# Optimization experiments

Measured on AMD Instinct MI355X. Metric: run time of the kernel, lower is better.

Reference implementation:

```python
import jax, jax.numpy as jnp
import numpy as np
from jax import lax

STRIDE = 2  # down_sample_stride
MATMUL_NORM = True


def maxpool2d_5d(x, s):
    # x: [B, T, C, H, W]; kernel=s, stride=s, padding=(s-1)//2 == 0 for s=2
    return lax.reduce_window(
        x, -jnp.inf, lax.max,
        window_dimensions=(1, 1, 1, s, s),
        window_strides=(1, 1, 1, s, s),
        padding='VALID')


def setup_inputs() -> dict:
    key = jax.random.key(0)
    k1, k2, k3, k4 = jax.random.split(key, 4)
    B, T, Ck, Cv, H, W = 2, 4, 64, 256, 64, 64
    return {
        'memory_keys': jax.random.normal(k1, (B, T, Ck, H, W), jnp.float32),
        'memory_values': jax.random.normal(k2, (B, T, Cv, H, W), jnp.float32),
        'query_key': jax.random.normal(k3, (B, Ck, H, W), jnp.float32),
        'query_value': jax.random.normal(k4, (B, Cv, H, W), jnp.float32),
    }


def reference(memory_keys, memory_values, query_key, query_value):
    B, T, Ck, oH, oW = memory_keys.shape
    Cv = memory_values.shape[2]
    # down-sample memory bank (max pool, stride 2, no padding)
    mk = maxpool2d_5d(memory_keys, STRIDE)   # [B,T,Ck,h,w]
    mv = maxpool2d_5d(memory_values, STRIDE) # [B,T,Cv,h,w]
    h, w = mk.shape[-2], mk.shape[-1]
    M = T * h * w
    N = oH * oH  # code uses ori_height*ori_height (square assumed)
    # permute(0,2,1,3,4).view(B,Ck,M).permute(0,2,1) -> [B, M, Ck]
    mk = mk.transpose(0, 2, 1, 3, 4).reshape(B, Ck, M).transpose(0, 2, 1)
    qk = query_key.reshape(B, Ck, N)
    attn = jnp.einsum('bmc,bcn->bmn', mk, qk)  # [B, M, N]
    if MATMUL_NORM:
        attn = attn * (Ck ** -0.5)
    attn = jax.nn.softmax(attn, axis=1)  # softmax over memory positions
    mv = mv.transpose(0, 2, 1, 3, 4).reshape(B, Cv, M)
    memory = jnp.einsum('bcm,bmn->bcn', mv, attn).reshape(B, Cv, oH, oW)
    return jnp.concatenate([query_value, memory], axis=1)  # [B, 2*Cv, H, W]
```

## Files before the change

### kernel.cpp

```cpp
#include <hip/hip_runtime.h>
#include <hip/hip_bf16.h>

typedef unsigned short u16;
typedef unsigned int   u32;
typedef __attribute__((ext_vector_type(8))) short  bf16x8;
typedef __attribute__((ext_vector_type(4))) float  floatx4;

#define NB 2
#define NT 4
#define CK 64
#define CV 256
#define HH 64
#define WW 64
#define MM 4096
#define NN 4096
#define SCALE 0.125f
#define SHIFT 4.0f
#define OUT_B 2097152
#define MSPLIT 2
#define MHALF 2048
#define ITERS 16

__device__ __forceinline__ u16 f2b(float f) {
    __hip_bfloat16 h = __float2bfloat16(f);
    union { __hip_bfloat16 h; u16 u; } v; v.h = h; return v.u;
}


#define KTOT (NB*MM*CK)
__global__ void pool_kv(const float* __restrict__ mk, const float* __restrict__ mv,
                        u16* __restrict__ pk, u16* __restrict__ vt) {
    int e = blockIdx.x * 256 + threadIdx.x;
    if (e < KTOT) {
        int m = e & 4095; int c = (e >> 12) & 63; int b = e >> 18;
        int ww = m & 31, hh = (m >> 5) & 31, t = m >> 10;
        const float* s = mk + ((size_t)(((b*NT + t)*CK + c)*HH + 2*hh))*WW + 2*ww;
        pk[((size_t)b*MM + m)*CK + c] =
            f2b(fmaxf(fmaxf(s[0], s[1]), fmaxf(s[WW], s[WW+1])));
    } else {
        int e2 = e - KTOT;
        int m = e2 & 4095; int c = (e2 >> 12) & 255; int b = e2 >> 20;
        int ww = m & 31, hh = (m >> 5) & 31, t = m >> 10;
        const float* s = mv + ((size_t)(((b*NT + t)*CV + c)*HH + 2*hh))*WW + 2*ww;
        vt[((size_t)b*CV + c)*MM + m] =
            f2b(fmaxf(fmaxf(s[0], s[1]), fmaxf(s[WW], s[WW+1])));
    }
}

__launch_bounds__(512)
__global__ void attn_mfma(const u16* __restrict__ pk, const u16* __restrict__ vt,
                          const float* __restrict__ qk,
                          float* __restrict__ part, float* __restrict__ sums) {
    const int ntile = blockIdx.x, b = blockIdx.y, ms = blockIdx.z;
    const int tid = threadIdx.x, w = tid >> 6, l = tid & 63;
    const int lrow = l & 15, quad = l >> 4;
    const int n0 = ntile * 64;
    const int m0 = ms * MHALF;

    __shared__ u16  P[64 * 128];
    __shared__ float sums_s[8][64];

    bf16x8 qf[2][4];
    const float* qb = qk + (size_t)b * CK * NN;
    #pragma unroll
    for (int cc = 0; cc < 2; ++cc)
        #pragma unroll
        for (int t = 0; t < 4; ++t) {
            int n = n0 + t*16 + lrow;
            #pragma unroll
            for (int i = 0; i < 8; ++i) {
                int c = cc*32 + quad*8 + i;
                qf[cc][t][i] = (short)f2b(qb[(size_t)c*NN + n]);
            }
        }

    const u16* pkb = pk + (size_t)b * MM * CK;
    const u16* vtb = vt + (size_t)b * CV * MM;

    floatx4 oacc[2][4];
    #pragma unroll
    for (int j = 0; j < 2; ++j)
        #pragma unroll
        for (int t = 0; t < 4; ++t)
            oacc[j][t] = (floatx4){0.f, 0.f, 0.f, 0.f};
    float sacc[4] = {0.f, 0.f, 0.f, 0.f};

    const int sw = lrow << 1;

    for (int it = 0; it < ITERS; ++it) {
        const int mbase = m0 + it * 128;

        const u16* kp = pkb + (size_t)(mbase + w*16 + lrow)*CK + quad*8;
        bf16x8 kf0 = *(const bf16x8*)(kp);
        bf16x8 kf1 = *(const bf16x8*)(kp + 32);

        bf16x8 vf[4][2];
        #pragma unroll
        for (int j = 0; j < 2; ++j) {
            const u16* vp = vtb + (size_t)(w*32 + j*16 + lrow)*MM + mbase + quad*8;
            vf[0][j] = *(const bf16x8*)(vp);
            vf[1][j] = *(const bf16x8*)(vp + 32);
            vf[2][j] = *(const bf16x8*)(vp + 64);
            vf[3][j] = *(const bf16x8*)(vp + 96);
        }

        #pragma unroll
        for (int t = 0; t < 4; ++t) {
            floatx4 s = __builtin_amdgcn_mfma_f32_16x16x32_bf16(
                            kf0, qf[0][t], (floatx4){0.f,0.f,0.f,0.f}, 0, 0, 0);
            s = __builtin_amdgcn_mfma_f32_16x16x32_bf16(kf1, qf[1][t], s, 0, 0, 0);
            float p0 = __expf(s[0]*SCALE - SHIFT);
            float p1 = __expf(s[1]*SCALE - SHIFT);
            float p2 = __expf(s[2]*SCALE - SHIFT);
            float p3 = __expf(s[3]*SCALE - SHIFT);
            sacc[t] += (p0 + p1) + (p2 + p3);
            u32 d0 = (u32)f2b(p0) | ((u32)f2b(p1) << 16);
            u32 d1 = (u32)f2b(p2) | ((u32)f2b(p3) << 16);
            int n_l = t*16 + lrow;
            int cb  = (w << 2) + quad;
            *(uint2*)&P[n_l*128 + ((cb ^ sw) << 2)] = make_uint2(d0, d1);
        }
        __syncthreads();

        #pragma unroll
        for (int cc = 0; cc < 4; ++cc) {
            bf16x8 pf[4];
            #pragma unroll
            for (int t = 0; t < 4; ++t) {
                int n_l = t*16 + lrow;
                int cb  = (cc << 3) + (quad << 1);
                pf[t] = *(const bf16x8*)&P[n_l*128 + ((cb ^ sw) << 2)];
            }
            #pragma unroll
            for (int j = 0; j < 2; ++j)
                #pragma unroll
                for (int t = 0; t < 4; ++t)
                    oacc[j][t] = __builtin_amdgcn_mfma_f32_16x16x32_bf16(
                                     vf[cc][j], pf[t], oacc[j][t], 0, 0, 0);
        }
        __syncthreads();
    }

    #pragma unroll
    for (int t = 0; t < 4; ++t) {
        float v = sacc[t];
        v += __shfl_xor(v, 16, 64);
        v += __shfl_xor(v, 32, 64);
        if (l < 16) sums_s[w][t*16 + l] = v;
    }
    __syncthreads();

    float* pb = part + ((size_t)((ms*NB + b)*64 + ntile)) * (256*64);
    #pragma unroll
    for (int j = 0; j < 2; ++j)
        #pragma unroll
        for (int t = 0; t < 4; ++t)
            #pragma unroll
            for (int r = 0; r < 4; ++r) {
                int c = w*32 + j*16 + quad*4 + r;
                int n = t*16 + lrow;
                pb[c*64 + n] = oacc[j][t][r];
            }
    if (tid < 64) {
        float sv = 0.f;
        #pragma unroll
        for (int ww2 = 0; ww2 < 8; ++ww2) sv += sums_s[ww2][tid];
        sums[((size_t)((ms*NB + b)*64 + ntile))*64 + tid] = sv;
    }
}

__global__ void epilogue(const float* __restrict__ part, const float* __restrict__ sums,
                         const float4* __restrict__ qv, float* __restrict__ out) {
    int e = blockIdx.x * 256 + threadIdx.x;
    if (e < 524288) {
        int b = e >> 18; int ru = e & 262143;
        ((float4*)out)[(size_t)b*(OUT_B/4) + ru] = qv[e];
    } else {
        int e4 = e - 524288;
        int nl4   = e4 & 15;
        int ntile = (e4 >> 4) & 63;
        int c     = (e4 >> 10) & 255;
        int b     = e4 >> 18;
        size_t t0 = (size_t)(0*NB + b)*64 + ntile;
        size_t t1 = (size_t)(1*NB + b)*64 + ntile;
        const float4* p4 = (const float4*)part;
        const float4* s4 = (const float4*)sums;
        float4 u0 = p4[t0*4096 + c*16 + nl4];
        float4 u1 = p4[t1*4096 + c*16 + nl4];
        float4 d0 = s4[t0*16 + nl4];
        float4 d1 = s4[t1*16 + nl4];
        float4 r;
        r.x = (u0.x + u1.x) / (d0.x + d1.x);
        r.y = (u0.y + u1.y) / (d0.y + d1.y);
        r.z = (u0.z + u1.z) / (d0.z + d1.z);
        r.w = (u0.w + u1.w) / (d0.w + d1.w);
        ((float4*)out)[(size_t)(b*512 + 256 + c)*1024 + ntile*16 + nl4] = r;
    }
}


__global__ void pool_v_f32(const float* __restrict__ src, float* __restrict__ out) {
    int e = blockIdx.x * 256 + threadIdx.x;
    int c = e & 255;
    int r = e >> 8;
    int ww = r & 31;  int hh = (r >> 5) & 31;
    int t  = (r >> 10) & 3;  int b = r >> 12;
    int m  = r & (MM - 1);
    const float* s = src + ((size_t)(((b*NT + t)*CV + c)*HH + 2*hh))*WW + 2*ww;
    out[(size_t)b*OUT_B + (size_t)m*CV + c] = fmaxf(fmaxf(s[0], s[1]), fmaxf(s[WW], s[WW+1]));
}

__global__ void pool_k_f32(const float* __restrict__ src, float* __restrict__ dst) {
    int e = blockIdx.x * 256 + threadIdx.x;
    int c = e & 63;
    int r = e >> 6;
    int ww = r & 31;  int hh = (r >> 5) & 31;
    int t  = (r >> 10) & 3;  int b = r >> 12;
    const float* s = src + ((size_t)(((b*NT + t)*CK + c)*HH + 2*hh))*WW + 2*ww;
    dst[e] = fmaxf(fmaxf(s[0], s[1]), fmaxf(s[WW], s[WW+1]));
}

__global__ void copy_qv_f32(const float4* __restrict__ src, float4* __restrict__ dst) {
    int u = blockIdx.x * 256 + threadIdx.x;
    int b  = u >> 18;
    int ru = u & 262143;
    dst[(size_t)b * (OUT_B/4) + ru] = src[u];
}

template<bool STAGED_K>
__launch_bounds__(256)
__global__ void attn_old(const float* __restrict__ pk,
                         const float* __restrict__ mk,
                         const float* __restrict__ qk,
                         float* __restrict__ out) {
    __shared__ __align__(16) float q_lds[CK][4];
    __shared__ __align__(16) float sarr[4][MM];
    __shared__ float inv_l[4];

    const int tid = threadIdx.x;
    const int blk = blockIdx.x;
    const int b   = blk >> 10;
    const int n0  = (blk & 1023) << 2;

    {
        int c = tid >> 2, qi = tid & 3;
        q_lds[c][qi] = qk[((size_t)(b*CK + c))*NN + n0 + qi];
    }
    __syncthreads();

    #pragma unroll
    for (int i = 0; i < 16; ++i) {
        int m = tid + (i << 8);
        float a0 = 0.f, a1 = 0.f, a2 = 0.f, a3 = 0.f;
        if (STAGED_K) {
            const float4* k4 = reinterpret_cast<const float4*>(pk + ((size_t)b*MM + m)*CK);
            #pragma unroll
            for (int cc = 0; cc < 16; ++cc) {
                float4 kv = k4[cc];
                int c = cc*4;
                float4 q0 = *reinterpret_cast<const float4*>(&q_lds[c][0]);
                float4 q1 = *reinterpret_cast<const float4*>(&q_lds[c+1][0]);
                float4 q2 = *reinterpret_cast<const float4*>(&q_lds[c+2][0]);
                float4 q3 = *reinterpret_cast<const float4*>(&q_lds[c+3][0]);
                a0 += kv.x*q0.x + kv.y*q1.x + kv.z*q2.x + kv.w*q3.x;
                a1 += kv.x*q0.y + kv.y*q1.y + kv.z*q2.y + kv.w*q3.y;
                a2 += kv.x*q0.z + kv.y*q1.z + kv.z*q2.z + kv.w*q3.z;
                a3 += kv.x*q0.w + kv.y*q1.w + kv.z*q2.w + kv.w*q3.w;
            }
        } else {
            int ww = m & 31, hh = (m >> 5) & 31, t = m >> 10;
            const float* base = mk + ((size_t)((b*NT + t)*CK)*HH + 2*hh)*WW + 2*ww;
            for (int c = 0; c < CK; ++c) {
                const float* s = base + (size_t)c*HH*WW;
                float kv = fmaxf(fmaxf(s[0], s[1]), fmaxf(s[WW], s[WW+1]));
                float4 q = *reinterpret_cast<const float4*>(&q_lds[c][0]);
                a0 += kv*q.x; a1 += kv*q.y; a2 += kv*q.z; a3 += kv*q.w;
            }
        }
        sarr[0][m] = a0*SCALE;
        sarr[1][m] = a1*SCALE;
        sarr[2][m] = a2*SCALE;
        sarr[3][m] = a3*SCALE;
    }
    __syncthreads();

    const int wave = tid >> 6, lane = tid & 63;
    float mx = -3.0e38f;
    for (int m = lane; m < MM; m += 64) mx = fmaxf(mx, sarr[wave][m]);
    #pragma unroll
    for (int off = 32; off > 0; off >>= 1) mx = fmaxf(mx, __shfl_xor(mx, off, 64));
    float ls = 0.f;
    for (int m = lane; m < MM; m += 64) {
        float p = __expf(sarr[wave][m] - mx);
        sarr[wave][m] = p;
        ls += p;
    }
    #pragma unroll
    for (int off = 32; off > 0; off >>= 1) ls += __shfl_xor(ls, off, 64);
    if (lane == 0) inv_l[wave] = 1.0f / ls;
    __syncthreads();

    const int c4 = lane;
    const float4* vb = reinterpret_cast<const float4*>(out + (size_t)b*OUT_B) + c4;
    const float* prow = sarr[wave];
    float a0 = 0.f, a1 = 0.f, a2 = 0.f, a3 = 0.f;
    for (int m = 0; m < MM; m += 4) {
        float4 p4 = *reinterpret_cast<const float4*>(prow + m);
        const float4* vp = vb + (size_t)m*(CV/4);
        float4 v0 = vp[0], v1 = vp[CV/4], v2 = vp[CV/2], v3 = vp[3*(CV/4)];
        a0 += p4.x*v0.x + p4.y*v1.x + p4.z*v2.x + p4.w*v3.x;
        a1 += p4.x*v0.y + p4.y*v1.y + p4.z*v2.y + p4.w*v3.y;
        a2 += p4.x*v0.z + p4.y*v1.z + p4.z*v2.z + p4.w*v3.z;
        a3 += p4.x*v0.w + p4.y*v1.w + p4.z*v2.w + p4.w*v3.w;
    }

    float inv = inv_l[wave];
    int n = n0 + wave;
    size_t ob = ((size_t)(b*512 + 256 + c4*4))*NN + n;
    out[ob]        = a0*inv;
    out[ob + NN]   = a1*inv;
    out[ob + 2*NN] = a2*inv;
    out[ob + 3*NN] = a3*inv;
}


extern "C" void kernel_launch(void* const* d_in, const int* in_sizes, int n_in,
                              void* d_out, int out_size, void* d_ws, size_t ws_size,
                              hipStream_t stream) {
    const float* mk = (const float*)d_in[0];
    const float* mv = (const float*)d_in[1];
    const float* qk = (const float*)d_in[2];
    const float* qv = (const float*)d_in[3];
    float* out = (float*)d_out;

    u16* pk_bf = (u16*)d_ws;
    u16* vt_bf = pk_bf + (size_t)NB*MM*CK;
    float* part = (float*)(vt_bf + (size_t)NB*CV*MM);
    float* sums = part + 4194304;
    const size_t need = (size_t)NB*MM*CK*2 + (size_t)NB*CV*MM*2
                      + (4194304 + 16384) * sizeof(float);

    if (ws_size >= need) {
        pool_kv<<<(KTOT + NB*MM*CV)/256, 256, 0, stream>>>(mk, mv, pk_bf, vt_bf);
        attn_mfma<<<dim3(64, NB, MSPLIT), 512, 0, stream>>>(pk_bf, vt_bf, qk, part, sums);
        epilogue<<<(2*524288)/256, 256, 0, stream>>>(part, sums, (const float4*)qv, out);
    } else {
        const size_t pk_bytes = (size_t)NB*MM*CK*sizeof(float);
        const bool staged = (ws_size >= pk_bytes);
        float* pk = (float*)d_ws;
        pool_v_f32<<<(NB*MM*CV)/256, 256, 0, stream>>>(mv, out);
        if (staged) {
            pool_k_f32<<<(NB*MM*CK)/256, 256, 0, stream>>>(mk, pk);
            attn_old<true ><<<NB*(NN/4), 256, 0, stream>>>(pk, mk, qk, out);
        } else {
            attn_old<false><<<NB*(NN/4), 256, 0, stream>>>(pk, mk, qk, out);
        }
        copy_qv_f32<<<((NB*CV*HH*WW)/4)/256, 256, 0, stream>>>((const float4*)qv, (float4*)out);
    }
}
```

Baseline: 148.2 us.

## Halve attention N-tile, double-buffer P in LDS, move query copy into pool kernel

The attention kernel now handles 32 query columns per block instead of 64, which doubles the grid to 512 blocks, and sets a launch-bounds occupancy hint of 4 blocks. The P tile in shared memory is double-buffered so the second barrier per iteration can be dropped, and V fragments are loaded inside the PV loop instead of being prefetched up front. These changes cut register pressure and give more parallelism. The query_value copy moves from the epilogue into the pooling kernel. In exchange, each V and K tile is reread by twice as many blocks, which adds global and L2 traffic.

```diff
diff --git a/kernel.cpp b/kernel.cpp
--- a/kernel.cpp
+++ b/kernel.cpp
@@ -27,9 +27,13 @@
 }
 
 
-#define KTOT (NB*MM*CK)
+#define KTOT 524288
+#define VTOT 2097152
+#define QTOT4 524288
 __global__ void pool_kv(const float* __restrict__ mk, const float* __restrict__ mv,
-                        u16* __restrict__ pk, u16* __restrict__ vt) {
+                        const float4* __restrict__ qv,
+                        u16* __restrict__ pk, u16* __restrict__ vt,
+                        float* __restrict__ out) {
     int e = blockIdx.x * 256 + threadIdx.x;
     if (e < KTOT) {
         int m = e & 4095; int c = (e >> 12) & 63; int b = e >> 18;
@@ -37,35 +41,39 @@
         const float* s = mk + ((size_t)(((b*NT + t)*CK + c)*HH + 2*hh))*WW + 2*ww;
         pk[((size_t)b*MM + m)*CK + c] =
             f2b(fmaxf(fmaxf(s[0], s[1]), fmaxf(s[WW], s[WW+1])));
-    } else {
+    } else if (e < KTOT + VTOT) {
         int e2 = e - KTOT;
         int m = e2 & 4095; int c = (e2 >> 12) & 255; int b = e2 >> 20;
         int ww = m & 31, hh = (m >> 5) & 31, t = m >> 10;
         const float* s = mv + ((size_t)(((b*NT + t)*CV + c)*HH + 2*hh))*WW + 2*ww;
         vt[((size_t)b*CV + c)*MM + m] =
             f2b(fmaxf(fmaxf(s[0], s[1]), fmaxf(s[WW], s[WW+1])));
-    }
-}
-
-__launch_bounds__(512)
+    } else {
+        int q = e - (KTOT + VTOT);
+        int b = q >> 18; int ru = q & 262143;
+        ((float4*)out)[(size_t)b*(OUT_B/4) + ru] = qv[q];
+    }
+}
+
+__launch_bounds__(512, 4)
 __global__ void attn_mfma(const u16* __restrict__ pk, const u16* __restrict__ vt,
                           const float* __restrict__ qk,
                           float* __restrict__ part, float* __restrict__ sums) {
     const int ntile = blockIdx.x, b = blockIdx.y, ms = blockIdx.z;
     const int tid = threadIdx.x, w = tid >> 6, l = tid & 63;
     const int lrow = l & 15, quad = l >> 4;
-    const int n0 = ntile * 64;
+    const int n0 = ntile * 32;
     const int m0 = ms * MHALF;
 
-    __shared__ u16  P[64 * 128];
-    __shared__ float sums_s[8][64];
-
-    bf16x8 qf[2][4];
+    __shared__ u16  P[2][32 * 128];
+    __shared__ float sums_s[8][32];
+
+    bf16x8 qf[2][2];
     const float* qb = qk + (size_t)b * CK * NN;
     #pragma unroll
     for (int cc = 0; cc < 2; ++cc)
         #pragma unroll
-        for (int t = 0; t < 4; ++t) {
+        for (int t = 0; t < 2; ++t) {
             int n = n0 + t*16 + lrow;
             #pragma unroll
             for (int i = 0; i < 8; ++i) {
@@ -77,35 +85,26 @@
     const u16* pkb = pk + (size_t)b * MM * CK;
     const u16* vtb = vt + (size_t)b * CV * MM;
 
-    floatx4 oacc[2][4];
+    floatx4 oacc[2][2];
     #pragma unroll
     for (int j = 0; j < 2; ++j)
         #pragma unroll
-        for (int t = 0; t < 4; ++t)
+        for (int t = 0; t < 2; ++t)
             oacc[j][t] = (floatx4){0.f, 0.f, 0.f, 0.f};
-    float sacc[4] = {0.f, 0.f, 0.f, 0.f};
+    float sacc[2] = {0.f, 0.f};
 
     const int sw = lrow << 1;
 
     for (int it = 0; it < ITERS; ++it) {
         const int mbase = m0 + it * 128;
+        u16* Pb = &P[it & 1][0];
 
         const u16* kp = pkb + (size_t)(mbase + w*16 + lrow)*CK + quad*8;
         bf16x8 kf0 = *(const bf16x8*)(kp);
         bf16x8 kf1 = *(const bf16x8*)(kp + 32);
 
-        bf16x8 vf[4][2];
-        #pragma unroll
-        for (int j = 0; j < 2; ++j) {
-            const u16* vp = vtb + (size_t)(w*32 + j*16 + lrow)*MM + mbase + quad*8;
-            vf[0][j] = *(const bf16x8*)(vp);
-            vf[1][j] = *(const bf16x8*)(vp + 32);
-            vf[2][j] = *(const bf16x8*)(vp + 64);
-            vf[3][j] = *(const bf16x8*)(vp + 96);
-        }
-
-        #pragma unroll
-        for (int t = 0; t < 4; ++t) {
+        #pragma unroll
+        for (int t = 0; t < 2; ++t) {
             floatx4 s = __builtin_amdgcn_mfma_f32_16x16x32_bf16(
                             kf0, qf[0][t], (floatx4){0.f,0.f,0.f,0.f}, 0, 0, 0);
             s = __builtin_amdgcn_mfma_f32_16x16x32_bf16(kf1, qf[1][t], s, 0, 0, 0);
@@ -118,31 +117,27 @@
             u32 d1 = (u32)f2b(p2) | ((u32)f2b(p3) << 16);
             int n_l = t*16 + lrow;
             int cb  = (w << 2) + quad;
-            *(uint2*)&P[n_l*128 + ((cb ^ sw) << 2)] = make_uint2(d0, d1);
+            *(uint2*)&Pb[n_l*128 + ((cb ^ sw) << 2)] = make_uint2(d0, d1);
         }
         __syncthreads();
 
         #pragma unroll
         for (int cc = 0; cc < 4; ++cc) {
-            bf16x8 pf[4];
-            #pragma unroll
-            for (int t = 0; t < 4; ++t) {
-                int n_l = t*16 + lrow;
-                int cb  = (cc << 3) + (quad << 1);
-                pf[t] = *(const bf16x8*)&P[n_l*128 + ((cb ^ sw) << 2)];
-            }
-            #pragma unroll
-            for (int j = 0; j < 2; ++j)
-                #pragma unroll
-                for (int t = 0; t < 4; ++t)
-                    oacc[j][t] = __builtin_amdgcn_mfma_f32_16x16x32_bf16(
-                                     vf[cc][j], pf[t], oacc[j][t], 0, 0, 0);
-        }
-        __syncthreads();
-    }
-
-    #pragma unroll
-    for (int t = 0; t < 4; ++t) {
+            const u16* vp = vtb + (size_t)(w*32 + lrow)*MM + mbase + cc*32 + quad*8;
+            bf16x8 vf0 = *(const bf16x8*)(vp);
+            bf16x8 vf1 = *(const bf16x8*)(vp + (size_t)16*MM);
+            int ch = (cc << 3) + (quad << 1);
+            bf16x8 pf0 = *(const bf16x8*)&Pb[(lrow     )*128 + ((ch ^ sw) << 2)];
+            bf16x8 pf1 = *(const bf16x8*)&Pb[(16 + lrow)*128 + ((ch ^ sw) << 2)];
+            oacc[0][0] = __builtin_amdgcn_mfma_f32_16x16x32_bf16(vf0, pf0, oacc[0][0], 0,0,0);
+            oacc[0][1] = __builtin_amdgcn_mfma_f32_16x16x32_bf16(vf0, pf1, oacc[0][1], 0,0,0);
+            oacc[1][0] = __builtin_amdgcn_mfma_f32_16x16x32_bf16(vf1, pf0, oacc[1][0], 0,0,0);
+            oacc[1][1] = __builtin_amdgcn_mfma_f32_16x16x32_bf16(vf1, pf1, oacc[1][1], 0,0,0);
+        }
+    }
+
+    #pragma unroll
+    for (int t = 0; t < 2; ++t) {
         float v = sacc[t];
         v += __shfl_xor(v, 16, 64);
         v += __shfl_xor(v, 32, 64);
@@ -150,52 +145,46 @@
     }
     __syncthreads();
 
-    float* pb = part + ((size_t)((ms*NB + b)*64 + ntile)) * (256*64);
+    float* pb = part + ((size_t)((ms*NB + b)*128 + ntile)) * (256*32);
     #pragma unroll
     for (int j = 0; j < 2; ++j)
         #pragma unroll
-        for (int t = 0; t < 4; ++t)
+        for (int t = 0; t < 2; ++t)
             #pragma unroll
             for (int r = 0; r < 4; ++r) {
                 int c = w*32 + j*16 + quad*4 + r;
                 int n = t*16 + lrow;
-                pb[c*64 + n] = oacc[j][t][r];
+                pb[c*32 + n] = oacc[j][t][r];
             }
-    if (tid < 64) {
+    if (tid < 32) {
         float sv = 0.f;
         #pragma unroll
         for (int ww2 = 0; ww2 < 8; ++ww2) sv += sums_s[ww2][tid];
-        sums[((size_t)((ms*NB + b)*64 + ntile))*64 + tid] = sv;
+        sums[((size_t)((ms*NB + b)*128 + ntile))*32 + tid] = sv;
     }
 }
 
 __global__ void epilogue(const float* __restrict__ part, const float* __restrict__ sums,
-                         const float4* __restrict__ qv, float* __restrict__ out) {
+                         float* __restrict__ out) {
     int e = blockIdx.x * 256 + threadIdx.x;
-    if (e < 524288) {
-        int b = e >> 18; int ru = e & 262143;
-        ((float4*)out)[(size_t)b*(OUT_B/4) + ru] = qv[e];
-    } else {
-        int e4 = e - 524288;
-        int nl4   = e4 & 15;
-        int ntile = (e4 >> 4) & 63;
-        int c     = (e4 >> 10) & 255;
-        int b     = e4 >> 18;
-        size_t t0 = (size_t)(0*NB + b)*64 + ntile;
-        size_t t1 = (size_t)(1*NB + b)*64 + ntile;
-        const float4* p4 = (const float4*)part;
-        const float4* s4 = (const float4*)sums;
-        float4 u0 = p4[t0*4096 + c*16 + nl4];
-        float4 u1 = p4[t1*4096 + c*16 + nl4];
-        float4 d0 = s4[t0*16 + nl4];
-        float4 d1 = s4[t1*16 + nl4];
-        float4 r;
-        r.x = (u0.x + u1.x) / (d0.x + d1.x);
-        r.y = (u0.y + u1.y) / (d0.y + d1.y);
-        r.z = (u0.z + u1.z) / (d0.z + d1.z);
-        r.w = (u0.w + u1.w) / (d0.w + d1.w);
-        ((float4*)out)[(size_t)(b*512 + 256 + c)*1024 + ntile*16 + nl4] = r;
-    }
+    int nl4   = e & 7;
+    int ntile = (e >> 3) & 127;
+    int c     = (e >> 10) & 255;
+    int b     = (e >> 18) & 1;
+    size_t t0 = (size_t)(0*NB + b)*128 + ntile;
+    size_t t1 = (size_t)(1*NB + b)*128 + ntile;
+    const float4* p4 = (const float4*)part;
+    const float4* s4 = (const float4*)sums;
+    float4 u0 = p4[t0*2048 + c*8 + nl4];
+    float4 u1 = p4[t1*2048 + c*8 + nl4];
+    float4 d0 = s4[t0*8 + nl4];
+    float4 d1 = s4[t1*8 + nl4];
+    float4 r;
+    r.x = (u0.x + u1.x) / (d0.x + d1.x);
+    r.y = (u0.y + u1.y) / (d0.y + d1.y);
+    r.z = (u0.z + u1.z) / (d0.z + d1.z);
+    r.w = (u0.w + u1.w) / (d0.w + d1.w);
+    ((float4*)out)[(size_t)(b*512 + 256 + c)*1024 + ntile*8 + nl4] = r;
 }
 
 
@@ -341,9 +330,10 @@
                       + (4194304 + 16384) * sizeof(float);
 
     if (ws_size >= need) {
-        pool_kv<<<(KTOT + NB*MM*CV)/256, 256, 0, stream>>>(mk, mv, pk_bf, vt_bf);
-        attn_mfma<<<dim3(64, NB, MSPLIT), 512, 0, stream>>>(pk_bf, vt_bf, qk, part, sums);
-        epilogue<<<(2*524288)/256, 256, 0, stream>>>(part, sums, (const float4*)qv, out);
+        pool_kv<<<(KTOT + VTOT + QTOT4)/256, 256, 0, stream>>>(mk, mv, (const float4*)qv,
+                                                               pk_bf, vt_bf, out);
+        attn_mfma<<<dim3(128, NB, MSPLIT), 512, 0, stream>>>(pk_bf, vt_bf, qk, part, sums);
+        epilogue<<<524288/256, 256, 0, stream>>>(part, sums, out);
     } else {
         const size_t pk_bytes = (size_t)NB*MM*CK*sizeof(float);
         const bool staged = (ws_size >= pk_bytes);
```

After: 176.4 us. +19.0%, slower.
